# Performance work log

Hardware: AMD Instinct MI355X
Metric: run time of the kernel (lower is better)

## Reference

```python
import jax, jax.numpy as jnp
import numpy as np

D_MODEL = 1024
D_STATE = 16
D_CONV = 4
EXPAND = 2
D_INNER = D_MODEL * EXPAND
B_SZ = 2
SEQ = 4096


def setup_inputs() -> dict:
    key = jax.random.key(0)
    ks = jax.random.split(key, 11)
    rn = lambda i, shape, scale=1.0: jax.random.normal(ks[i], shape, jnp.float32) * scale
    return {
        "x": rn(0, (B_SZ, SEQ, D_MODEL)),
        "W_in": rn(1, (D_MODEL, D_INNER), D_MODEL ** -0.5),
        "b_in": rn(2, (D_INNER,), 0.01),
        "conv_w": rn(3, (D_INNER, 1, D_CONV), 0.1),   # torch depthwise layout [out_ch, in_ch/groups=1, k]
        "conv_b": rn(4, (D_INNER,), 0.01),
        # A scaled so tanh(A) is contractive -> stable recurrence over 4096 steps
        "A": rn(5, (D_STATE, D_STATE), 0.1),
        "Bp": rn(6, (D_STATE,)),   # B parameter [d_state, 1] flattened
        "Cp": rn(7, (D_STATE,)),   # C parameter [1, d_state] flattened
        "Dp": rn(8, (1,)),
        "W_out": rn(9, (D_INNER, D_MODEL), D_INNER ** -0.5),
        "b_out": rn(10, (D_MODEL,), 0.01),
    }


def reference(x, W_in, b_in, conv_w, conv_b, A, Bp, Cp, Dp, W_out, b_out):
    Bsz, S, _ = x.shape
    d_inner = W_in.shape[1]
    # input projection
    u = x @ W_in + b_in                              # [B, S, d_inner]
    # causal depthwise conv (torch pads k-1 both sides then slices [:S])
    u = u.transpose(0, 2, 1)                         # [B, d_inner, S]
    u = jax.lax.conv_general_dilated(
        u, conv_w, window_strides=(1,), padding=[(D_CONV - 1, 0)],
        dimension_numbers=("NCH", "OIH", "NCH"),
        feature_group_count=d_inner) + conv_b[None, :, None]
    u = u.transpose(0, 2, 1)                         # [B, S, d_inner]
    # per-channel scalar SSM shared across channels: h_t = tanh(A) h_{t-1} + B u_t; y_t = C h_t + D u_t
    At = jnp.tanh(A)                                 # [ds, ds]
    def step(h, u_t):                                # h: [B, d_inner, ds], u_t: [B, d_inner]
        h = jnp.einsum("ij,bdj->bdi", At, h) + u_t[..., None] * Bp
        y = jnp.einsum("j,bdj->bd", Cp, h) + Dp[0] * u_t
        return h, y
    h0 = jnp.zeros((Bsz, d_inner, Bp.shape[0]), x.dtype)
    _, ys = jax.lax.scan(step, h0, u.transpose(1, 0, 2))  # ys: [S, B, d_inner]
    y = jax.nn.silu(ys.transpose(1, 0, 2))           # [B, S, d_inner]
    return y @ W_out + b_out                         # [B, S, d_model]
```

## Files before the change

### kernel.cpp

```cpp
#include <hip/hip_runtime.h>

typedef unsigned short u16;
typedef float  f32x4  __attribute__((ext_vector_type(4)));
typedef __bf16 bf16x8 __attribute__((ext_vector_type(8)));
typedef u16    u16x2  __attribute__((ext_vector_type(2)));
typedef u16    u16x4  __attribute__((ext_vector_type(4)));

#define D_MODEL 1024
#define D_INNER 2048
#define B_SZ    2
#define SEQ     4096
#define MROWS   (B_SZ * SEQ)
#define LTAPS   64
#define KFIR    192
#define CVROW   200

__device__ __forceinline__ u16 f2bf(float f) {
    return __builtin_bit_cast(u16, (__bf16)f);
}
__device__ __forceinline__ float bf2f(u16 h) {
    unsigned u = ((unsigned)h) << 16;
    return __builtin_bit_cast(float, u);
}

typedef __attribute__((address_space(1))) void gv_t;
typedef __attribute__((address_space(3))) void lv_t;
__device__ __forceinline__ void glds16(const u16* g, u16* l) {
    __builtin_amdgcn_global_load_lds((gv_t*)g, (lv_t*)l, 16, 0, 0);
}
#define WAIT_VM0   0x0F70
#define WAIT_VM4   0x0F74
#define WAIT_LGKM0 0xC07F
#define SCHED_FENCE() asm volatile("" ::: "memory")

__device__ __forceinline__ void transpose_tile(
    const float* __restrict__ in, u16* __restrict__ out,
    int R, int C, int c0, int r0, int tid, float (*tile)[33])
{
    const int tx = tid & 31, ty = tid >> 5;
    for (int k = 0; k < 32; k += 8)
        tile[ty + k][tx] = in[(size_t)(r0 + ty + k) * C + c0 + tx];
    __syncthreads();
    for (int k = 0; k < 32; k += 8)
        out[(size_t)(c0 + ty + k) * R + r0 + tx] = f2bf(tile[tx][ty + k]);
}

__global__ __launch_bounds__(256) void prep_kernel(
    const float* __restrict__ x, u16* __restrict__ xb,
    const float* __restrict__ Win, u16* __restrict__ WinT,
    const float* __restrict__ Wout, u16* __restrict__ WoutT,
    const float* __restrict__ A, const float* __restrict__ Bp,
    const float* __restrict__ Cp, const float* __restrict__ Dp,
    u16* __restrict__ Amat192)
{
    __shared__ float tile[32][33];
    __shared__ float fs[LTAPS];
    const int bx = blockIdx.x, tid = threadIdx.x;
    if (bx < 8192) {
        size_t i = ((size_t)bx * 256 + tid) * 4;
        f32x4 v = *(const f32x4*)(x + i);
        u16x4 o;
        o.x = f2bf(v.x); o.y = f2bf(v.y); o.z = f2bf(v.z); o.w = f2bf(v.w);
        *(u16x4*)(xb + i) = o;
    } else if (bx < 10240) {
        const int flat = bx - 8192;
        transpose_tile(Win, WinT, 1024, 2048,
                       (flat & 63) * 32, (flat >> 6) * 32, tid, tile);
    } else if (bx < 12288) {
        const int flat = bx - 10240;
        transpose_tile(Wout, WoutT, 2048, 1024,
                       (flat & 31) * 32, (flat >> 5) * 32, tid, tile);
    } else {
        if (tid < 64) {
            const int i = tid & 15;
            float Atr[16];
            for (int j = 0; j < 16; j++) Atr[j] = tanhf(A[i * 16 + j]);
            float p = Bp[i];
            const float c  = Cp[i];
            const float d0 = Dp[0];
            for (int t = 0; t < LTAPS; t++) {
                float fv = c * p;
                fv += __shfl_xor(fv, 1); fv += __shfl_xor(fv, 2);
                fv += __shfl_xor(fv, 4); fv += __shfl_xor(fv, 8);
                if (tid == 0) fs[t] = fv + (t == 0 ? d0 : 0.f);
                float n0 = 0.f, n1 = 0.f, n2 = 0.f, n3 = 0.f;
                #pragma unroll
                for (int j = 0; j < 4; j++) {
                    n0 = fmaf(Atr[j],      __shfl(p, j),      n0);
                    n1 = fmaf(Atr[j + 4],  __shfl(p, j + 4),  n1);
                    n2 = fmaf(Atr[j + 8],  __shfl(p, j + 8),  n2);
                    n3 = fmaf(Atr[j + 12], __shfl(p, j + 12), n3);
                }
                p = (n0 + n1) + (n2 + n3);
            }
        }
        __syncthreads();
        for (int idx = tid; idx < 128 * KFIR; idx += 256) {
            const int i = idx / KFIR, j = idx % KFIR;
            const int tau = 64 + i - j;
            float v = (tau >= 0 && tau < LTAPS) ? fs[tau] : 0.f;
            Amat192[idx] = f2bf(v);
        }
    }
}

template <int MODE>
__global__ __launch_bounds__(256) void gemm_bt_kernel(
    const u16* __restrict__ A, const u16* __restrict__ BT,
    void* __restrict__ Cout, const float* __restrict__ bias,
    int M, int N, int K)
{
    __shared__ u16 As[2][128 * 32];
    __shared__ u16 Bs[2][128 * 32];
    const int tid = threadIdx.x, lane = tid & 63, wid = tid >> 6;
    const int nTiles = gridDim.x;
    const int bid = blockIdx.x + nTiles * blockIdx.y;
    const int xcd = bid & 7;
    const int loc = bid >> 3;
    const int mt  = xcd * (gridDim.y >> 3) + (loc & 7);
    const int nt  = loc >> 3;
    const int m0 = mt * 128, n0 = nt * 128;
    const int sr = wid * 32 + (lane >> 2);
    const int sc = (lane & 3) * 8;
    const u16* ga = A  + (size_t)(m0 + sr) * K + sc;
    const u16* gb = BT + (size_t)(n0 + sr) * K + sc;
    const int lo = wid * 1024;
    const int wm = (wid & 1) * 64, wn = (wid >> 1) * 64;
    const int fr = lane & 15, fq = lane >> 4;
    f32x4 acc[4][4] = {};
    glds16(ga,                    As[0] + lo);
    glds16(ga + (size_t)16 * K,   As[0] + lo + 512);
    glds16(gb,                    Bs[0] + lo);
    glds16(gb + (size_t)16 * K,   Bs[0] + lo + 512);
    glds16(ga + 32,               As[1] + lo);
    glds16(ga + 32 + (size_t)16 * K, As[1] + lo + 512);
    glds16(gb + 32,               Bs[1] + lo);
    glds16(gb + 32 + (size_t)16 * K, Bs[1] + lo + 512);
    const int iters = K >> 5;
    for (int it = 0; it < iters; ++it) {
        if (it + 1 < iters) __builtin_amdgcn_s_waitcnt(WAIT_VM4);
        else                __builtin_amdgcn_s_waitcnt(WAIT_VM0);
        __builtin_amdgcn_s_barrier();
        SCHED_FENCE();
        const u16* Ab = As[it & 1];
        const u16* Bb = Bs[it & 1];
        bf16x8 af[4], bfr[4];
        #pragma unroll
        for (int i = 0; i < 4; i++)
            af[i]  = *(const bf16x8*)(Ab + (wm + i * 16 + fr) * 32 + fq * 8);
        #pragma unroll
        for (int i = 0; i < 4; i++)
            bfr[i] = *(const bf16x8*)(Bb + (wn + i * 16 + fr) * 32 + fq * 8);
        SCHED_FENCE();
        __builtin_amdgcn_s_waitcnt(WAIT_LGKM0);
        __builtin_amdgcn_s_barrier();
        SCHED_FENCE();
        if (it + 2 < iters) {
            const int k0 = (it + 2) << 5;
            u16* la = As[it & 1] + lo;
            u16* lb = Bs[it & 1] + lo;
            glds16(ga + k0,                  la);
            glds16(ga + k0 + (size_t)16 * K, la + 512);
            glds16(gb + k0,                  lb);
            glds16(gb + k0 + (size_t)16 * K, lb + 512);
        }
        #pragma unroll
        for (int mi = 0; mi < 4; mi++)
            #pragma unroll
            for (int ni = 0; ni < 4; ni++)
                acc[mi][ni] = __builtin_amdgcn_mfma_f32_16x16x32_bf16(
                    bfr[ni], af[mi], acc[mi][ni], 0, 0, 0);
    }
    for (int ni = 0; ni < 4; ni++) {
        const int colb = n0 + wn + ni * 16 + fq * 4;
        const f32x4 bv = *(const f32x4*)(bias + colb);
        for (int mi = 0; mi < 4; mi++) {
            const int row = m0 + wm + mi * 16 + fr;
            f32x4 v = acc[mi][ni];
            v.x += bv.x; v.y += bv.y; v.z += bv.z; v.w += bv.w;
            if constexpr (MODE == 0) {
                u16x4 o;
                o.x = f2bf(v.x); o.y = f2bf(v.y); o.z = f2bf(v.z); o.w = f2bf(v.w);
                *(u16x4*)((u16*)Cout + (size_t)row * N + colb) = o;
            } else {
                *(f32x4*)((float*)Cout + (size_t)row * N + colb) = v;
            }
        }
    }
}

__global__ __launch_bounds__(256) void conv_fir_mfma_kernel(
    const u16* __restrict__ u, const float* __restrict__ cw,
    const float* __restrict__ cb, const u16* __restrict__ Amat192,
    u16* __restrict__ Y)
{
    __shared__ u16 VT[128 * CVROW];
    const int tid = threadIdx.x;
    const int c0 = blockIdx.x * 128, t0 = blockIdx.y * 128, b = blockIdx.z;
    {
        const int tx = tid & 63, ty = tid >> 6;
        const int cg = c0 + tx * 2;
        const f32x4 wA = *(const f32x4*)(cw + cg * 4);
        const f32x4 wB = *(const f32x4*)(cw + cg * 4 + 4);
        const float cb0 = cb[cg], cb1 = cb[cg + 1];
        const u16* ucol = u + (size_t)b * SEQ * D_INNER + cg;
        const int sbase = t0 - 64 + ty * 48;
        u16* vr0 = VT + (tx * 2)     * CVROW + ty * 48;
        u16* vr1 = VT + (tx * 2 + 1) * CVROW + ty * 48;
        float am3 = 0.f, am2 = 0.f, am1 = 0.f;
        float bm3 = 0.f, bm2 = 0.f, bm1 = 0.f;
        if (sbase > 0) {
            u16x2 d3 = *(const u16x2*)(ucol + (size_t)(sbase - 3) * D_INNER);
            u16x2 d2 = *(const u16x2*)(ucol + (size_t)(sbase - 2) * D_INNER);
            u16x2 d1 = *(const u16x2*)(ucol + (size_t)(sbase - 1) * D_INNER);
            am3 = bf2f(d3.x); bm3 = bf2f(d3.y);
            am2 = bf2f(d2.x); bm2 = bf2f(d2.y);
            am1 = bf2f(d1.x); bm1 = bf2f(d1.y);
        }
        #pragma unroll 4
        for (int j = 0; j < 12; j++) {
            const int sq = sbase + j * 4;
            if (sq < 0) {
                const u16x4 z = {0, 0, 0, 0};
                *(u16x4*)(vr0 + j * 4) = z;
                *(u16x4*)(vr1 + j * 4) = z;
            } else {
                const u16* p = ucol + (size_t)sq * D_INNER;
                u16x2 r0 = *(const u16x2*)(p);
                u16x2 r1 = *(const u16x2*)(p + (size_t)D_INNER);
                u16x2 r2 = *(const u16x2*)(p + (size_t)2 * D_INNER);
                u16x2 r3 = *(const u16x2*)(p + (size_t)3 * D_INNER);
                float a0 = bf2f(r0.x), b0 = bf2f(r0.y);
                float a1 = bf2f(r1.x), b1 = bf2f(r1.y);
                float a2 = bf2f(r2.x), b2 = bf2f(r2.y);
                float a3 = bf2f(r3.x), b3 = bf2f(r3.y);
                u16x4 oa, ob;
                oa.x = f2bf(cb0 + wA.x * am3 + wA.y * am2 + wA.z * am1 + wA.w * a0);
                oa.y = f2bf(cb0 + wA.x * am2 + wA.y * am1 + wA.z * a0  + wA.w * a1);
                oa.z = f2bf(cb0 + wA.x * am1 + wA.y * a0  + wA.z * a1  + wA.w * a2);
                oa.w = f2bf(cb0 + wA.x * a0  + wA.y * a1  + wA.z * a2  + wA.w * a3);
                ob.x = f2bf(cb1 + wB.x * bm3 + wB.y * bm2 + wB.z * bm1 + wB.w * b0);
                ob.y = f2bf(cb1 + wB.x * bm2 + wB.y * bm1 + wB.z * b0  + wB.w * b1);
                ob.z = f2bf(cb1 + wB.x * bm1 + wB.y * b0  + wB.z * b1  + wB.w * b2);
                ob.w = f2bf(cb1 + wB.x * b0  + wB.y * b1  + wB.z * b2  + wB.w * b3);
                *(u16x4*)(vr0 + j * 4) = oa;
                *(u16x4*)(vr1 + j * 4) = ob;
                am3 = a1; am2 = a2; am1 = a3;
                bm3 = b1; bm2 = b2; bm1 = b3;
            }
        }
    }
    __syncthreads();
    const int lane = tid & 63, wid = tid >> 6;
    const int wm = (wid & 1) * 64, wn = (wid >> 1) * 64;
    const int fr = lane & 15, fq = lane >> 4;
    f32x4 acc[4][4] = {};
    #pragma unroll
    for (int kq = 0; kq < 6; kq++) {
        const int k0 = kq * 32;
        bf16x8 af[4], bfr[4];
        #pragma unroll
        for (int mi = 0; mi < 4; mi++)
            af[mi] = *(const bf16x8*)(Amat192 + (wm + mi * 16 + fr) * KFIR + k0 + fq * 8);
        #pragma unroll
        for (int ni = 0; ni < 4; ni++)
            bfr[ni] = *(const bf16x8*)(VT + (wn + ni * 16 + fr) * CVROW + k0 + fq * 8);
        #pragma unroll
        for (int mi = 0; mi < 4; mi++)
            #pragma unroll
            for (int ni = 0; ni < 4; ni++)
                acc[mi][ni] = __builtin_amdgcn_mfma_f32_16x16x32_bf16(
                    bfr[ni], af[mi], acc[mi][ni], 0, 0, 0);
    }
    #pragma unroll
    for (int ni = 0; ni < 4; ni++) {
        const int cbase = c0 + wn + ni * 16 + fq * 4;
        #pragma unroll
        for (int mi = 0; mi < 4; mi++) {
            const int trow = t0 + wm + mi * 16 + fr;
            f32x4 v = acc[mi][ni];
            u16x4 o;
            o.x = f2bf(v.x / (1.f + __expf(-v.x)));
            o.y = f2bf(v.y / (1.f + __expf(-v.y)));
            o.z = f2bf(v.z / (1.f + __expf(-v.z)));
            o.w = f2bf(v.w / (1.f + __expf(-v.w)));
            *(u16x4*)(Y + ((size_t)(b * SEQ + trow)) * D_INNER + cbase) = o;
        }
    }
}

extern "C" void kernel_launch(void* const* d_in, const int* in_sizes, int n_in,
                              void* d_out, int out_size, void* d_ws, size_t ws_size,
                              hipStream_t stream)
{
    const float* x    = (const float*)d_in[0];
    const float* Win  = (const float*)d_in[1];
    const float* bin  = (const float*)d_in[2];
    const float* cw   = (const float*)d_in[3];
    const float* cb   = (const float*)d_in[4];
    const float* A    = (const float*)d_in[5];
    const float* Bp   = (const float*)d_in[6];
    const float* Cp   = (const float*)d_in[7];
    const float* Dp   = (const float*)d_in[8];
    const float* Wout = (const float*)d_in[9];
    const float* bout = (const float*)d_in[10];
    float* out = (float*)d_out;

    char* ws = (char*)d_ws;
    u16* xb      = (u16*)(ws);
    u16* WinT    = (u16*)(ws + 16777216);
    u16* WoutT   = (u16*)(ws + 20971520);
    u16* u       = (u16*)(ws + 25165824);
    u16* Y       = (u16*)(ws + 58720256);
    u16* Amat192 = (u16*)(ws + 92274688);

    prep_kernel<<<12289, 256, 0, stream>>>(x, xb, Win, WinT, Wout, WoutT,
                                           A, Bp, Cp, Dp, Amat192);
    gemm_bt_kernel<0><<<dim3(16, 64), 256, 0, stream>>>(xb, WinT, u, bin,
                                                        MROWS, D_INNER, D_MODEL);
    conv_fir_mfma_kernel<<<dim3(16, 32, 2), 256, 0, stream>>>(u, cw, cb, Amat192, Y);
    gemm_bt_kernel<1><<<dim3(8, 64), 256, 0, stream>>>(Y, WoutT, out, bout,
                                                       MROWS, D_MODEL, D_INNER);
}
```

Measured before the change: 257.5 us.

## Emit channel-major u from input GEMM and use BK=64 single-buffered GEMM tiles

```diff
diff --git a/kernel.cpp b/kernel.cpp
--- a/kernel.cpp
+++ b/kernel.cpp
@@ -3,8 +3,8 @@
 typedef unsigned short u16;
 typedef float  f32x4  __attribute__((ext_vector_type(4)));
 typedef __bf16 bf16x8 __attribute__((ext_vector_type(8)));
-typedef u16    u16x2  __attribute__((ext_vector_type(2)));
 typedef u16    u16x4  __attribute__((ext_vector_type(4)));
+typedef u16    u16x8  __attribute__((ext_vector_type(8)));
 
 #define D_MODEL 1024
 #define D_INNER 2048
@@ -29,7 +29,6 @@
     __builtin_amdgcn_global_load_lds((gv_t*)g, (lv_t*)l, 16, 0, 0);
 }
 #define WAIT_VM0   0x0F70
-#define WAIT_VM4   0x0F74
 #define WAIT_LGKM0 0xC07F
 #define SCHED_FENCE() asm volatile("" ::: "memory")
 
@@ -104,80 +103,83 @@
     }
 }
 
-template <int MODE>
+template <int MODE, bool BIAS_M>
 __global__ __launch_bounds__(256) void gemm_bt_kernel(
     const u16* __restrict__ A, const u16* __restrict__ BT,
     void* __restrict__ Cout, const float* __restrict__ bias,
     int M, int N, int K)
 {
-    __shared__ u16 As[2][128 * 32];
-    __shared__ u16 Bs[2][128 * 32];
+    __shared__ u16 As[128 * 64];
+    __shared__ u16 Bs[128 * 64];
     const int tid = threadIdx.x, lane = tid & 63, wid = tid >> 6;
     const int nTiles = gridDim.x;
     const int bid = blockIdx.x + nTiles * blockIdx.y;
     const int xcd = bid & 7;
     const int loc = bid >> 3;
-    const int mt  = xcd * (gridDim.y >> 3) + (loc & 7);
-    const int nt  = loc >> 3;
+    const int strip = gridDim.y >> 3;
+    const int mt  = xcd * strip + (loc & (strip - 1));
+    const int nt  = loc / strip;
     const int m0 = mt * 128, n0 = nt * 128;
-    const int sr = wid * 32 + (lane >> 2);
-    const int sc = (lane & 3) * 8;
+    const int sr = wid * 32 + (lane >> 3);
+    const int sc = (lane & 7) * 8;
     const u16* ga = A  + (size_t)(m0 + sr) * K + sc;
     const u16* gb = BT + (size_t)(n0 + sr) * K + sc;
-    const int lo = wid * 1024;
+    u16* la = As + wid * 2048;
+    u16* lb = Bs + wid * 2048;
     const int wm = (wid & 1) * 64, wn = (wid >> 1) * 64;
     const int fr = lane & 15, fq = lane >> 4;
     f32x4 acc[4][4] = {};
-    glds16(ga,                    As[0] + lo);
-    glds16(ga + (size_t)16 * K,   As[0] + lo + 512);
-    glds16(gb,                    Bs[0] + lo);
-    glds16(gb + (size_t)16 * K,   Bs[0] + lo + 512);
-    glds16(ga + 32,               As[1] + lo);
-    glds16(ga + 32 + (size_t)16 * K, As[1] + lo + 512);
-    glds16(gb + 32,               Bs[1] + lo);
-    glds16(gb + 32 + (size_t)16 * K, Bs[1] + lo + 512);
-    const int iters = K >> 5;
+    #pragma unroll
+    for (int r = 0; r < 32; r += 8) {
+        glds16(ga + (size_t)r * K, la + r * 64);
+        glds16(gb + (size_t)r * K, lb + r * 64);
+    }
+    const int iters = K >> 6;
     for (int it = 0; it < iters; ++it) {
-        if (it + 1 < iters) __builtin_amdgcn_s_waitcnt(WAIT_VM4);
-        else                __builtin_amdgcn_s_waitcnt(WAIT_VM0);
+        __builtin_amdgcn_s_waitcnt(WAIT_VM0);
         __builtin_amdgcn_s_barrier();
         SCHED_FENCE();
-        const u16* Ab = As[it & 1];
-        const u16* Bb = Bs[it & 1];
-        bf16x8 af[4], bfr[4];
+        bf16x8 af[4][2], bfr[4][2];
         #pragma unroll
         for (int i = 0; i < 4; i++)
-            af[i]  = *(const bf16x8*)(Ab + (wm + i * 16 + fr) * 32 + fq * 8);
-        #pragma unroll
-        for (int i = 0; i < 4; i++)
-            bfr[i] = *(const bf16x8*)(Bb + (wn + i * 16 + fr) * 32 + fq * 8);
+            #pragma unroll
+            for (int kk = 0; kk < 2; kk++) {
+                af[i][kk]  = *(const bf16x8*)(As + (wm + i * 16 + fr) * 64 + kk * 32 + fq * 8);
+                bfr[i][kk] = *(const bf16x8*)(Bs + (wn + i * 16 + fr) * 64 + kk * 32 + fq * 8);
+            }
         SCHED_FENCE();
         __builtin_amdgcn_s_waitcnt(WAIT_LGKM0);
         __builtin_amdgcn_s_barrier();
         SCHED_FENCE();
-        if (it + 2 < iters) {
-            const int k0 = (it + 2) << 5;
-            u16* la = As[it & 1] + lo;
-            u16* lb = Bs[it & 1] + lo;
-            glds16(ga + k0,                  la);
-            glds16(ga + k0 + (size_t)16 * K, la + 512);
-            glds16(gb + k0,                  lb);
-            glds16(gb + k0 + (size_t)16 * K, lb + 512);
-        }
-        #pragma unroll
-        for (int mi = 0; mi < 4; mi++)
+        if (it + 1 < iters) {
+            const int k0 = (it + 1) << 6;
             #pragma unroll
-            for (int ni = 0; ni < 4; ni++)
-                acc[mi][ni] = __builtin_amdgcn_mfma_f32_16x16x32_bf16(
-                    bfr[ni], af[mi], acc[mi][ni], 0, 0, 0);
-    }
-    for (int ni = 0; ni < 4; ni++) {
-        const int colb = n0 + wn + ni * 16 + fq * 4;
-        const f32x4 bv = *(const f32x4*)(bias + colb);
-        for (int mi = 0; mi < 4; mi++) {
-            const int row = m0 + wm + mi * 16 + fr;
+            for (int r = 0; r < 32; r += 8) {
+                glds16(ga + k0 + (size_t)r * K, la + r * 64);
+                glds16(gb + k0 + (size_t)r * K, lb + r * 64);
+            }
+        }
+        #pragma unroll
+        for (int kk = 0; kk < 2; kk++)
+            #pragma unroll
+            for (int mi = 0; mi < 4; mi++)
+                #pragma unroll
+                for (int ni = 0; ni < 4; ni++)
+                    acc[mi][ni] = __builtin_amdgcn_mfma_f32_16x16x32_bf16(
+                        bfr[ni][kk], af[mi][kk], acc[mi][ni], 0, 0, 0);
+    }
+    for (int mi = 0; mi < 4; mi++) {
+        const int row = m0 + wm + mi * 16 + fr;
+        const float bm = BIAS_M ? bias[row] : 0.f;
+        for (int ni = 0; ni < 4; ni++) {
+            const int colb = n0 + wn + ni * 16 + fq * 4;
             f32x4 v = acc[mi][ni];
-            v.x += bv.x; v.y += bv.y; v.z += bv.z; v.w += bv.w;
+            if constexpr (BIAS_M) {
+                v.x += bm; v.y += bm; v.z += bm; v.w += bm;
+            } else {
+                const f32x4 bv = *(const f32x4*)(bias + colb);
+                v.x += bv.x; v.y += bv.y; v.z += bv.z; v.w += bv.w;
+            }
             if constexpr (MODE == 0) {
                 u16x4 o;
                 o.x = f2bf(v.x); o.y = f2bf(v.y); o.z = f2bf(v.z); o.w = f2bf(v.w);
@@ -190,7 +192,7 @@
 }
 
 __global__ __launch_bounds__(256) void conv_fir_mfma_kernel(
-    const u16* __restrict__ u, const float* __restrict__ cw,
+    const u16* __restrict__ uT, const float* __restrict__ cw,
     const float* __restrict__ cb, const u16* __restrict__ Amat192,
     u16* __restrict__ Y)
 {
@@ -198,56 +200,41 @@
     const int tid = threadIdx.x;
     const int c0 = blockIdx.x * 128, t0 = blockIdx.y * 128, b = blockIdx.z;
     {
-        const int tx = tid & 63, ty = tid >> 6;
-        const int cg = c0 + tx * 2;
-        const f32x4 wA = *(const f32x4*)(cw + cg * 4);
-        const f32x4 wB = *(const f32x4*)(cw + cg * 4 + 4);
-        const float cb0 = cb[cg], cb1 = cb[cg + 1];
-        const u16* ucol = u + (size_t)b * SEQ * D_INNER + cg;
-        const int sbase = t0 - 64 + ty * 48;
-        u16* vr0 = VT + (tx * 2)     * CVROW + ty * 48;
-        u16* vr1 = VT + (tx * 2 + 1) * CVROW + ty * 48;
-        float am3 = 0.f, am2 = 0.f, am1 = 0.f;
-        float bm3 = 0.f, bm2 = 0.f, bm1 = 0.f;
-        if (sbase > 0) {
-            u16x2 d3 = *(const u16x2*)(ucol + (size_t)(sbase - 3) * D_INNER);
-            u16x2 d2 = *(const u16x2*)(ucol + (size_t)(sbase - 2) * D_INNER);
-            u16x2 d1 = *(const u16x2*)(ucol + (size_t)(sbase - 1) * D_INNER);
-            am3 = bf2f(d3.x); bm3 = bf2f(d3.y);
-            am2 = bf2f(d2.x); bm2 = bf2f(d2.y);
-            am1 = bf2f(d1.x); bm1 = bf2f(d1.y);
-        }
-        #pragma unroll 4
-        for (int j = 0; j < 12; j++) {
-            const int sq = sbase + j * 4;
-            if (sq < 0) {
-                const u16x4 z = {0, 0, 0, 0};
-                *(u16x4*)(vr0 + j * 4) = z;
-                *(u16x4*)(vr1 + j * 4) = z;
+        const int tx = tid & 127, ty = tid >> 7;
+        const int c = c0 + tx;
+        const f32x4 w = *(const f32x4*)(cw + c * 4);
+        const float cbv = cb[c];
+        const u16* urow = uT + (size_t)c * MROWS + (size_t)b * SEQ;
+        const int j0 = ty * 96;
+        const int s0 = t0 - 64 + j0;
+        u16* vdst = VT + tx * CVROW + j0;
+        float xm3 = 0.f, xm2 = 0.f, xm1 = 0.f;
+        if (s0 > 0) {
+            xm3 = bf2f(urow[s0 - 3]);
+            xm2 = bf2f(urow[s0 - 2]);
+            xm1 = bf2f(urow[s0 - 1]);
+        }
+        #pragma unroll
+        for (int jj = 0; jj < 96; jj += 8) {
+            const int s = s0 + jj;
+            u16x8 o;
+            if (s < 0) {
+                #pragma unroll
+                for (int q = 0; q < 8; q++) o[q] = 0;
             } else {
-                const u16* p = ucol + (size_t)sq * D_INNER;
-                u16x2 r0 = *(const u16x2*)(p);
-                u16x2 r1 = *(const u16x2*)(p + (size_t)D_INNER);
-                u16x2 r2 = *(const u16x2*)(p + (size_t)2 * D_INNER);
-                u16x2 r3 = *(const u16x2*)(p + (size_t)3 * D_INNER);
-                float a0 = bf2f(r0.x), b0 = bf2f(r0.y);
-                float a1 = bf2f(r1.x), b1 = bf2f(r1.y);
-                float a2 = bf2f(r2.x), b2 = bf2f(r2.y);
-                float a3 = bf2f(r3.x), b3 = bf2f(r3.y);
-                u16x4 oa, ob;
-                oa.x = f2bf(cb0 + wA.x * am3 + wA.y * am2 + wA.z * am1 + wA.w * a0);
-                oa.y = f2bf(cb0 + wA.x * am2 + wA.y * am1 + wA.z * a0  + wA.w * a1);
-                oa.z = f2bf(cb0 + wA.x * am1 + wA.y * a0  + wA.z * a1  + wA.w * a2);
-                oa.w = f2bf(cb0 + wA.x * a0  + wA.y * a1  + wA.z * a2  + wA.w * a3);
-                ob.x = f2bf(cb1 + wB.x * bm3 + wB.y * bm2 + wB.z * bm1 + wB.w * b0);
-                ob.y = f2bf(cb1 + wB.x * bm2 + wB.y * bm1 + wB.z * b0  + wB.w * b1);
-                ob.z = f2bf(cb1 + wB.x * bm1 + wB.y * b0  + wB.z * b1  + wB.w * b2);
-                ob.w = f2bf(cb1 + wB.x * b0  + wB.y * b1  + wB.z * b2  + wB.w * b3);
-                *(u16x4*)(vr0 + j * 4) = oa;
-                *(u16x4*)(vr1 + j * 4) = ob;
-                am3 = a1; am2 = a2; am1 = a3;
-                bm3 = b1; bm2 = b2; bm1 = b3;
-            }
+                u16x8 r = *(const u16x8*)(urow + s);
+                float xv[8];
+                #pragma unroll
+                for (int q = 0; q < 8; q++) xv[q] = bf2f(r[q]);
+                o[0] = f2bf(cbv + w.x * xm3   + w.y * xm2   + w.z * xm1   + w.w * xv[0]);
+                o[1] = f2bf(cbv + w.x * xm2   + w.y * xm1   + w.z * xv[0] + w.w * xv[1]);
+                o[2] = f2bf(cbv + w.x * xm1   + w.y * xv[0] + w.z * xv[1] + w.w * xv[2]);
+                #pragma unroll
+                for (int q = 3; q < 8; q++)
+                    o[q] = f2bf(cbv + w.x * xv[q-3] + w.y * xv[q-2] + w.z * xv[q-1] + w.w * xv[q]);
+                xm3 = xv[5]; xm2 = xv[6]; xm1 = xv[7];
+            }
+            *(u16x8*)(vdst + jj) = o;
         }
     }
     __syncthreads();
@@ -310,15 +297,15 @@
     u16* xb      = (u16*)(ws);
     u16* WinT    = (u16*)(ws + 16777216);
     u16* WoutT   = (u16*)(ws + 20971520);
-    u16* u       = (u16*)(ws + 25165824);
+    u16* uT      = (u16*)(ws + 25165824);
     u16* Y       = (u16*)(ws + 58720256);
     u16* Amat192 = (u16*)(ws + 92274688);
 
     prep_kernel<<<12289, 256, 0, stream>>>(x, xb, Win, WinT, Wout, WoutT,
                                            A, Bp, Cp, Dp, Amat192);
-    gemm_bt_kernel<0><<<dim3(16, 64), 256, 0, stream>>>(xb, WinT, u, bin,
-                                                        MROWS, D_INNER, D_MODEL);
-    conv_fir_mfma_kernel<<<dim3(16, 32, 2), 256, 0, stream>>>(u, cw, cb, Amat192, Y);
-    gemm_bt_kernel<1><<<dim3(8, 64), 256, 0, stream>>>(Y, WoutT, out, bout,
-                                                       MROWS, D_MODEL, D_INNER);
-}
+    gemm_bt_kernel<0, true><<<dim3(64, 16), 256, 0, stream>>>(
+        WinT, xb, uT, bin, D_INNER, MROWS, D_MODEL);
+    conv_fir_mfma_kernel<<<dim3(16, 32, 2), 256, 0, stream>>>(uT, cw, cb, Amat192, Y);
+    gemm_bt_kernel<1, false><<<dim3(8, 64), 256, 0, stream>>>(
+        Y, WoutT, out, bout, MROWS, D_MODEL, D_INNER);
+}
```

Measured after the change: 266.0 us. 3.3% more time.
